# Optimization experiments

Measured on AMD Instinct MI355X. Metric: run time of the kernel, lower is better.

Reference implementation:

```python
import jax, jax.numpy as jnp
import numpy as np

K_NUM = 4      # kernel_num: size of dynamic kernel bank
KS = 3         # spatial kernel size


def _fdconv(x, w_fr, w_fi, b, a1w, a1b, a2w, a2b):
    """Frequency-dynamic conv: kernels parameterized in the Fourier domain,
    mixed per-sample by a GAP->MLP->softmax attention over the kernel bank,
    then applied as a per-sample 3x3 conv (batched via grouped conv).
    x: [B,Cin,H,W]; w_fr/w_fi: [K,Cout,Cin,3,2] (rfft2 coeffs); b: [Cout]."""
    B, Cin, H, W = x.shape
    # per-sample kernel attention
    gap = x.mean((2, 3))                                   # [B,Cin]
    h = jax.nn.relu(gap @ a1w + a1b)                       # [B,hidden]
    attn = jax.nn.softmax(h @ a2w + a2b, axis=-1)          # [B,K]
    # synthesize spatial kernels from frequency coefficients
    w = jnp.fft.irfft2(w_fr + 1j * w_fi, s=(KS, KS), axes=(-2, -1))  # [K,Co,Ci,3,3]
    w = w.astype(x.dtype)
    wd = jnp.einsum('bk,koihw->boihw', attn, w)            # [B,Co,Ci,3,3]
    Co = wd.shape[1]
    # per-sample conv via feature_group_count=B grouped conv
    xg = x.reshape(1, B * Cin, H, W)
    wg = wd.reshape(B * Co, Cin, KS, KS)
    y = jax.lax.conv_general_dilated(
        xg, wg, window_strides=(1, 1), padding='SAME',
        dimension_numbers=('NCHW', 'OIHW', 'NCHW'),
        feature_group_count=B)
    return y.reshape(B, Co, H, W) + b[None, :, None, None]


def setup_inputs() -> dict:
    key = jax.random.key(0)
    ks = jax.random.split(key, 16)
    B, Cin, Cout, H, W = 16, 128, 256, 128, 128
    h1, h2 = Cin // 4, Cout // 4
    FR = KS // 2 + 1  # rfft bins along last dim
    s = 0.05
    return {
        'x': jax.random.normal(ks[0], (B, Cin, H, W), jnp.float32),
        # conv1 (Cin->Cout)
        'w1_fr': jax.random.normal(ks[1], (K_NUM, Cout, Cin, KS, FR), jnp.float32) * s,
        'w1_fi': jax.random.normal(ks[2], (K_NUM, Cout, Cin, KS, FR), jnp.float32) * s,
        'b1': jnp.zeros((Cout,), jnp.float32),
        'a1w1': jax.random.normal(ks[3], (Cin, h1), jnp.float32) * s,
        'a1b1': jnp.zeros((h1,), jnp.float32),
        'a1w2': jax.random.normal(ks[4], (h1, K_NUM), jnp.float32) * s,
        'a1b2': jnp.zeros((K_NUM,), jnp.float32),
        # conv2 (Cout->Cout)
        'w2_fr': jax.random.normal(ks[5], (K_NUM, Cout, Cout, KS, FR), jnp.float32) * s,
        'w2_fi': jax.random.normal(ks[6], (K_NUM, Cout, Cout, KS, FR), jnp.float32) * s,
        'b2': jnp.zeros((Cout,), jnp.float32),
        'a2w1': jax.random.normal(ks[7], (Cout, h2), jnp.float32) * s,
        'a2b1': jnp.zeros((h2,), jnp.float32),
        'a2w2': jax.random.normal(ks[8], (h2, K_NUM), jnp.float32) * s,
        'a2b2': jnp.zeros((K_NUM,), jnp.float32),
    }


def reference(x, w1_fr, w1_fi, b1, a1w1, a1b1, a1w2, a1b2,
              w2_fr, w2_fi, b2, a2w1, a2b1, a2w2, a2b2):
    y = jax.nn.relu(_fdconv(x, w1_fr, w1_fi, b1, a1w1, a1b1, a1w2, a1b2))
    y = jax.nn.relu(_fdconv(y, w2_fr, w2_fi, b2, a2w1, a2b1, a2w2, a2b2))
    return y
```

## Files before the change

### kernel.cpp

```cpp
#include <hip/hip_runtime.h>
#include <hip/hip_bf16.h>
#include <math.h>


#define K_NUM 4
typedef __attribute__((ext_vector_type(8))) short short8;
typedef __attribute__((ext_vector_type(4))) float f32x4;

__device__ inline float bf2f(short s) {
  unsigned u = ((unsigned)(unsigned short)s) << 16;
  return __uint_as_float(u);
}
__device__ inline short f2bf(float f) {
  __hip_bfloat16 h = __float2bfloat16(f);
  return (short)*reinterpret_cast<unsigned short*>(&h);
}

__global__ __launch_bounds__(256) void gap_reduce_kernel(
    const float* __restrict__ part, float* __restrict__ gap, float scale, int n4) {
  int row = blockIdx.x * 4 + (threadIdx.x >> 6);
  int lane = threadIdx.x & 63;
  float4 v = {0.f, 0.f, 0.f, 0.f};
  if (lane < n4) v = *(const float4*)(part + (size_t)row * 256 + lane * 4);
  float s = v.x + v.y + v.z + v.w;
#pragma unroll
  for (int m = 1; m <= 32; m <<= 1) s += __shfl_xor(s, m, 64);
  if (lane == 0) gap[row] = s * scale;
}

__global__ void fd_attn_kernel(const float* __restrict__ gap, int C, int Hd,
                               const float* __restrict__ w1, const float* __restrict__ b1,
                               const float* __restrict__ w2, const float* __restrict__ b2,
                               float* __restrict__ attn) {
  int b = blockIdx.x, j = threadIdx.x;
  __shared__ float h[64];
  __shared__ float z[K_NUM];
  if (j < Hd) {
    float s = b1[j];
    const float* g = gap + (size_t)b * C;
    for (int c = 0; c < C; ++c) s = fmaf(g[c], w1[c * Hd + j], s);
    h[j] = fmaxf(s, 0.f);
  }
  __syncthreads();
  if (j < K_NUM) {
    float s = b2[j];
    for (int c = 0; c < Hd; ++c) s = fmaf(h[c], w2[c * K_NUM + j], s);
    z[j] = s;
  }
  __syncthreads();
  if (j == 0) {
    float m = z[0];
    for (int k = 1; k < K_NUM; ++k) m = fmaxf(m, z[k]);
    float e[K_NUM], sum = 0.f;
    for (int k = 0; k < K_NUM; ++k) { e[k] = expf(z[k] - m); sum += e[k]; }
    for (int k = 0; k < K_NUM; ++k) attn[b * K_NUM + k] = e[k] / sum;
  }
}

__global__ void fd_synth_t_kernel(const float* __restrict__ wfr, const float* __restrict__ wfi,
                                  const float* __restrict__ attn, short* __restrict__ wdt,
                                  int B, int CO, int CI) {
  size_t gid = (size_t)blockIdx.x * blockDim.x + threadIdx.x;
  size_t total = (size_t)B * CI * CO;
  if (gid >= total) return;
  int ci = (int)(gid % CI);
  size_t t = gid / CI;
  int co = (int)(t % CO);
  int b = (int)(t / CO);

  float a[K_NUM];
  for (int k = 0; k < K_NUM; ++k) a[k] = attn[b * K_NUM + k];

  float Fr[3][2], Fi[3][2];
  for (int u = 0; u < 3; ++u) for (int v = 0; v < 2; ++v) { Fr[u][v] = 0.f; Fi[u][v] = 0.f; }
  for (int k = 0; k < K_NUM; ++k) {
    size_t base = ((((size_t)k * CO + co) * CI + ci) * 3) * 2;
    const float* pr = wfr + base;
    const float* pi = wfi + base;
    float ak = a[k];
    for (int u = 0; u < 3; ++u)
      for (int v = 0; v < 2; ++v) {
        Fr[u][v] = fmaf(ak, pr[u * 2 + v], Fr[u][v]);
        Fi[u][v] = fmaf(ak, pi[u * 2 + v], Fi[u][v]);
      }
  }

  const float CS[3] = {1.f, -0.5f, -0.5f};
  const float SN[3] = {0.f, 0.8660254037844386f, -0.8660254037844386f};
  float outv[9];
  for (int ai = 0; ai < 3; ++ai) {
    float Gr[2], Gi[2];
    for (int v = 0; v < 2; ++v) {
      float gr = 0.f, gi = 0.f;
      for (int u = 0; u < 3; ++u) {
        int idx = (u * ai) % 3;
        gr += Fr[u][v] * CS[idx] - Fi[u][v] * SN[idx];
        gi += Fr[u][v] * SN[idx] + Fi[u][v] * CS[idx];
      }
      Gr[v] = gr * (1.f / 3.f);
      Gi[v] = gi * (1.f / 3.f);
    }
    for (int bi = 0; bi < 3; ++bi)
      outv[ai * 3 + bi] = (Gr[0] + 2.f * (Gr[1] * CS[bi] - Gi[1] * SN[bi])) * (1.f / 3.f);
  }
  int ci8 = ci >> 3, cil = ci & 7;
  for (int s = 0; s < 9; ++s)
    wdt[((((size_t)b * 9 + s) * (CI / 8) + ci8) * CO + co) * 8 + cil] = f2bf(outv[s]);
}

__global__ __launch_bounds__(256) void transpose_bf16_kernel(
    const float* __restrict__ in, short* __restrict__ out, int C,
    float* __restrict__ gpart1) {
  const int HW = 16384;
  __shared__ short t[64 * 40];
  int tid = threadIdx.x;
  int px0 = blockIdx.x * 64, c0 = blockIdx.y * 32, b = blockIdx.z;
  int px = tid & 63, cb = tid >> 6;
  float sums[8];
#pragma unroll
  for (int i = 0; i < 8; ++i) {
    int c = i * 4 + cb;
    float v = in[((size_t)b * C + c0 + c) * HW + px0 + px];
    t[px * 40 + c] = f2bf(v);
    sums[i] = v;
  }
  __syncthreads();
  int px2 = tid >> 2, g = tid & 3;
  short8 v = *(const short8*)(t + px2 * 40 + g * 8);
  *(short8*)(out + ((size_t)b * HW + px0 + px2) * C + c0 + g * 8) = v;
#pragma unroll
  for (int m = 1; m <= 32; m <<= 1)
#pragma unroll
    for (int i = 0; i < 8; ++i) sums[i] += __shfl_xor(sums[i], m, 64);
  if ((tid & 63) == 0)
#pragma unroll
    for (int i = 0; i < 8; ++i)
      gpart1[((size_t)b * C + c0 + i * 4 + cb) * 256 + blockIdx.x] = sums[i];
}

template <int CI, int MODE>
__global__ __launch_bounds__(512, 2) void conv_mfma_kernel(
    const short* __restrict__ xin,
    const short* __restrict__ wdt,
    const float* __restrict__ bias,
    short* __restrict__ yout_t,
    float* __restrict__ yout_f,
    float* __restrict__ gpart2) {
  const int H = 128, W = 128, HW = H * W, CO = 256;
  const int NKC = CI / 32;
  __shared__ short xs[2][18 * 18 * 40];

  const int tid = threadIdx.x;
  const int w = tid >> 6;
  const int wy = w & 1, wc = w >> 1;
  const int lane = tid & 63;
  const int l15 = lane & 15, l4 = lane >> 4;
  const int tx0 = (blockIdx.x & 7) * 16, ty0 = (blockIdx.x >> 3) * 16;
  const int cob = wc * 64;
  const int b = blockIdx.z;

  int sr[3], sc[3], sg[3];
#pragma unroll
  for (int i = 0; i < 3; ++i) {
    int idx = i * 512 + tid;
    int pxi = idx >> 2;
    sg[i] = idx & 3;
    sr[i] = pxi / 18;
    sc[i] = pxi - sr[i] * 18;
  }
  const bool has2 = (tid < 272);

  short8 pre[3];
  auto stage_load = [&](int kc) {
#pragma unroll
    for (int i = 0; i < 3; ++i) {
      if (i < 2 || has2) {
        int gy = ty0 + sr[i] - 1, gx = tx0 + sc[i] - 1;
        short8 v = {0, 0, 0, 0, 0, 0, 0, 0};
        if ((unsigned)gy < (unsigned)H && (unsigned)gx < (unsigned)W)
          v = *(const short8*)(xin + ((size_t)b * HW + gy * W + gx) * CI + kc * 32 + sg[i] * 8);
        pre[i] = v;
      }
    }
  };
  auto stage_write = [&](short* buf) {
#pragma unroll
    for (int i = 0; i < 3; ++i) {
      if (i < 2 || has2) {
        int pxi = sr[i] * 18 + sc[i];
        *(short8*)(buf + pxi * 40 + sg[i] * 8) = pre[i];
      }
    }
  };

  f32x4 acc[8][4];
#pragma unroll
  for (int i = 0; i < 8; ++i)
#pragma unroll
    for (int j = 0; j < 4; ++j)
      acc[i][j] = (f32x4){0.f, 0.f, 0.f, 0.f};

  stage_load(0);
  stage_write(xs[0]);
  __syncthreads();

  int cur = 0;
  for (int kc = 0; kc < NKC; ++kc) {
    const bool more = (kc + 1 < NKC);
    if (more) stage_load(kc + 1);
    const short* bufc = xs[cur];

#pragma unroll
    for (int dc = 0; dc < 3; ++dc) {
      short8 xf[10];
#pragma unroll
      for (int rr = 0; rr < 10; ++rr)
        xf[rr] = *(const short8*)(bufc + ((8 * wy + rr) * 18 + l15 + dc) * 40 + l4 * 8);
#pragma unroll
      for (int dr = 0; dr < 3; ++dr) {
        short8 wf[4];
        const short* wp = wdt + ((((size_t)b * 9 + dr * 3 + dc) * (CI / 8) + kc * 4 + l4) * CO + cob + l15) * 8;
#pragma unroll
        for (int cf = 0; cf < 4; ++cf)
          wf[cf] = *(const short8*)(wp + cf * 128);
#pragma unroll
        for (int nf = 0; nf < 8; ++nf)
#pragma unroll
          for (int cf = 0; cf < 4; ++cf) {
            if (MODE == 0)
              acc[nf][cf] = __builtin_amdgcn_mfma_f32_16x16x32_bf16(
                  xf[nf + dr], wf[cf], acc[nf][cf], 0, 0, 0);
            else
              acc[nf][cf] = __builtin_amdgcn_mfma_f32_16x16x32_bf16(
                  wf[cf], xf[nf + dr], acc[nf][cf], 0, 0, 0);
          }
      }
    }

    if (more) stage_write(xs[cur ^ 1]);
    __syncthreads();
    cur ^= 1;
  }

  if (MODE == 0) {
    float gs[4];
#pragma unroll
    for (int cf = 0; cf < 4; ++cf) gs[cf] = 0.f;
#pragma unroll
    for (int cf = 0; cf < 4; ++cf) {
      float bs = bias[cob + cf * 16 + l15];
#pragma unroll
      for (int nf = 0; nf < 8; ++nf) {
        int row = ty0 + 8 * wy + nf;
#pragma unroll
        for (int r = 0; r < 4; ++r) {
          int col = tx0 + l4 * 4 + r;
          float v = fmaxf(acc[nf][cf][r] + bs, 0.f);
          gs[cf] += v;
          yout_t[((size_t)b * HW + (size_t)row * W + col) * CO + cob + cf * 16 + l15] = f2bf(v);
        }
      }
    }
#pragma unroll
    for (int cf = 0; cf < 4; ++cf) {
      gs[cf] += __shfl_xor(gs[cf], 16, 64);
      gs[cf] += __shfl_xor(gs[cf], 32, 64);
    }
    if (l4 == 0) {
      int pslot = blockIdx.x * 2 + wy;
#pragma unroll
      for (int cf = 0; cf < 4; ++cf)
        gpart2[((size_t)b * 256 + cob + cf * 16 + l15) * 256 + pslot] = gs[cf];
    }
  } else {
#pragma unroll
    for (int cf = 0; cf < 4; ++cf) {
#pragma unroll
      for (int r = 0; r < 4; ++r) {
        int co = cob + cf * 16 + l4 * 4 + r;
        float bs = bias[co];
#pragma unroll
        for (int nf = 0; nf < 8; ++nf) {
          int row = ty0 + 8 * wy + nf;
          int col = tx0 + l15;
          yout_f[((size_t)b * CO + co) * HW + (size_t)row * W + col] =
              fmaxf(acc[nf][cf][r] + bs, 0.f);
        }
      }
    }
  }
}

extern "C" void kernel_launch(void* const* d_in, const int* in_sizes, int n_in,
                              void* d_out, int out_size, void* d_ws, size_t ws_size,
                              hipStream_t stream) {
  const int B = 16, CIN = 128, COUT = 256, H = 128, W = 128, HW = H * W;

  const float* x    = (const float*)d_in[0];
  const float* w1fr = (const float*)d_in[1];
  const float* w1fi = (const float*)d_in[2];
  const float* b1   = (const float*)d_in[3];
  const float* a1w1 = (const float*)d_in[4];
  const float* a1b1 = (const float*)d_in[5];
  const float* a1w2 = (const float*)d_in[6];
  const float* a1b2 = (const float*)d_in[7];
  const float* w2fr = (const float*)d_in[8];
  const float* w2fi = (const float*)d_in[9];
  const float* b2   = (const float*)d_in[10];
  const float* a2w1 = (const float*)d_in[11];
  const float* a2b1 = (const float*)d_in[12];
  const float* a2w2 = (const float*)d_in[13];
  const float* a2b2 = (const float*)d_in[14];
  float* outf = (float*)d_out;

  short* xt     = (short*)d_out;
  float* gpart1 = (float*)((char*)d_out + 67108864);
  float* gpart2 = (float*)((char*)d_out + 69206016);

  char* wsb = (char*)d_ws;
  short* y1t  = (short*)wsb;
  short* wdt  = (short*)(wsb + 134217728);
  float* gap1 = (float*)(wsb + 134217728 + 18874368);
  float* gap2 = (float*)(wsb + 134217728 + 18874368 + 8192);
  float* attn = (float*)(wsb + 134217728 + 18874368 + 8192 + 16384);

  const float gsc = 1.f / (float)HW;

  transpose_bf16_kernel<<<dim3(HW / 64, CIN / 32, B), 256, 0, stream>>>(x, xt, CIN, gpart1);
  gap_reduce_kernel<<<(B * CIN) / 4, 256, 0, stream>>>(gpart1, gap1, gsc, 64);
  fd_attn_kernel<<<B, 64, 0, stream>>>(gap1, CIN, CIN / 4, a1w1, a1b1, a1w2, a1b2, attn);
  fd_synth_t_kernel<<<(B * CIN * COUT) / 256, 256, 0, stream>>>(w1fr, w1fi, attn, wdt, B, COUT, CIN);
  conv_mfma_kernel<128, 0><<<dim3(64, 1, 16), 512, 0, stream>>>(xt, wdt, b1, y1t, nullptr, gpart2);

  gap_reduce_kernel<<<(B * COUT) / 4, 256, 0, stream>>>(gpart2, gap2, gsc, 32);
  fd_attn_kernel<<<B, 64, 0, stream>>>(gap2, COUT, COUT / 4, a2w1, a2b1, a2w2, a2b2, attn);
  fd_synth_t_kernel<<<(B * COUT * COUT) / 256, 256, 0, stream>>>(w2fr, w2fi, attn, wdt, B, COUT, COUT);
  conv_mfma_kernel<256, 1><<<dim3(64, 1, 16), 512, 0, stream>>>(y1t, wdt, b2, nullptr, outf, nullptr);
}
```

Baseline: 925.6 us.

## Switch conv to 32x32x16 MFMA with 32x8 tiles and channel-group-major LDS layout

Reworks the per-sample conv kernel to use 32x32x16 bf16 MFMA instead of 16x16x32. The spatial tile changes from 16x16 to 32 wide by 8 high. Shared memory becomes channel-group-major with a padded pixel stride, and staging is simplified to one pixel per thread. The larger MFMA shape is meant to raise operand reuse and cut LDS reads and issue overhead per FLOP. In exchange, the halo overhead of the wider, shorter tile grows, and the new LDS pattern may cause bank conflicts.

After: 1.015 ms. +9.6%, slower.

```diff
diff --git a/kernel.cpp b/kernel.cpp
--- a/kernel.cpp
+++ b/kernel.cpp
@@ -6,6 +6,7 @@
 #define K_NUM 4
 typedef __attribute__((ext_vector_type(8))) short short8;
 typedef __attribute__((ext_vector_type(4))) float f32x4;
+typedef __attribute__((ext_vector_type(16))) float f32x16;
 
 __device__ inline float bf2f(short s) {
   unsigned u = ((unsigned)(unsigned short)s) << 16;
@@ -148,57 +149,51 @@
     float* __restrict__ gpart2) {
   const int H = 128, W = 128, HW = H * W, CO = 256;
   const int NKC = CI / 32;
-  __shared__ short xs[2][18 * 18 * 40];
+  const int NPX = 340;
+  const int NPXP = 346;
+  __shared__ short xs[2][4 * NPXP * 8];
 
   const int tid = threadIdx.x;
   const int w = tid >> 6;
   const int wy = w & 1, wc = w >> 1;
   const int lane = tid & 63;
-  const int l15 = lane & 15, l4 = lane >> 4;
-  const int tx0 = (blockIdx.x & 7) * 16, ty0 = (blockIdx.x >> 3) * 16;
+  const int l31 = lane & 31;
+  const int h = lane >> 5;
+  const int tx0 = (blockIdx.x & 3) * 32, ty0 = (blockIdx.x >> 2) * 8;
   const int cob = wc * 64;
   const int b = blockIdx.z;
 
-  int sr[3], sc[3], sg[3];
-#pragma unroll
-  for (int i = 0; i < 3; ++i) {
-    int idx = i * 512 + tid;
-    int pxi = idx >> 2;
-    sg[i] = idx & 3;
-    sr[i] = pxi / 18;
-    sc[i] = pxi - sr[i] * 18;
-  }
-  const bool has2 = (tid < 272);
-
-  short8 pre[3];
+  const int sp = tid;
+  const int srr = sp / 34, scc = sp - srr * 34;
+  const int sgy = ty0 + srr - 1, sgx = tx0 + scc - 1;
+  const bool sok = (tid < NPX);
+  const bool sin = sok && (unsigned)sgy < (unsigned)H && (unsigned)sgx < (unsigned)W;
+  const short* sgp = xin + ((size_t)b * HW + sgy * W + sgx) * CI;
+
+  short8 pre[4];
   auto stage_load = [&](int kc) {
 #pragma unroll
-    for (int i = 0; i < 3; ++i) {
-      if (i < 2 || has2) {
-        int gy = ty0 + sr[i] - 1, gx = tx0 + sc[i] - 1;
-        short8 v = {0, 0, 0, 0, 0, 0, 0, 0};
-        if ((unsigned)gy < (unsigned)H && (unsigned)gx < (unsigned)W)
-          v = *(const short8*)(xin + ((size_t)b * HW + gy * W + gx) * CI + kc * 32 + sg[i] * 8);
-        pre[i] = v;
-      }
+    for (int g = 0; g < 4; ++g) {
+      short8 v = {0, 0, 0, 0, 0, 0, 0, 0};
+      if (sin) v = *(const short8*)(sgp + kc * 32 + g * 8);
+      pre[g] = v;
     }
   };
   auto stage_write = [&](short* buf) {
-#pragma unroll
-    for (int i = 0; i < 3; ++i) {
-      if (i < 2 || has2) {
-        int pxi = sr[i] * 18 + sc[i];
-        *(short8*)(buf + pxi * 40 + sg[i] * 8) = pre[i];
-      }
+    if (sok) {
+#pragma unroll
+      for (int g = 0; g < 4; ++g)
+        *(short8*)(buf + (g * NPXP + sp) * 8) = pre[g];
     }
   };
 
-  f32x4 acc[8][4];
-#pragma unroll
-  for (int i = 0; i < 8; ++i)
-#pragma unroll
-    for (int j = 0; j < 4; ++j)
-      acc[i][j] = (f32x4){0.f, 0.f, 0.f, 0.f};
+  f32x16 acc[4][2];
+#pragma unroll
+  for (int i = 0; i < 4; ++i)
+#pragma unroll
+    for (int j = 0; j < 2; ++j)
+#pragma unroll
+      for (int r = 0; r < 16; ++r) acc[i][j][r] = 0.f;
 
   stage_load(0);
   stage_write(xs[0]);
@@ -212,28 +207,33 @@
 
 #pragma unroll
     for (int dc = 0; dc < 3; ++dc) {
-      short8 xf[10];
-#pragma unroll
-      for (int rr = 0; rr < 10; ++rr)
-        xf[rr] = *(const short8*)(bufc + ((8 * wy + rr) * 18 + l15 + dc) * 40 + l4 * 8);
-#pragma unroll
-      for (int dr = 0; dr < 3; ++dr) {
-        short8 wf[4];
-        const short* wp = wdt + ((((size_t)b * 9 + dr * 3 + dc) * (CI / 8) + kc * 4 + l4) * CO + cob + l15) * 8;
-#pragma unroll
-        for (int cf = 0; cf < 4; ++cf)
-          wf[cf] = *(const short8*)(wp + cf * 128);
-#pragma unroll
-        for (int nf = 0; nf < 8; ++nf)
-#pragma unroll
-          for (int cf = 0; cf < 4; ++cf) {
-            if (MODE == 0)
-              acc[nf][cf] = __builtin_amdgcn_mfma_f32_16x16x32_bf16(
-                  xf[nf + dr], wf[cf], acc[nf][cf], 0, 0, 0);
-            else
-              acc[nf][cf] = __builtin_amdgcn_mfma_f32_16x16x32_bf16(
-                  wf[cf], xf[nf + dr], acc[nf][cf], 0, 0, 0);
-          }
+#pragma unroll
+      for (int ks = 0; ks < 2; ++ks) {
+        short8 xf[6];
+#pragma unroll
+        for (int rr = 0; rr < 6; ++rr) {
+          int p = (wy * 4 + rr) * 34 + l31 + dc;
+          xf[rr] = *(const short8*)(bufc + ((ks * 2 + h) * NPXP + p) * 8);
+        }
+#pragma unroll
+        for (int dr = 0; dr < 3; ++dr) {
+          short8 wf[2];
+          const short* wp = wdt + ((((size_t)b * 9 + dr * 3 + dc) * (CI / 8) + kc * 4 + ks * 2 + h) * CO + cob + l31) * 8;
+#pragma unroll
+          for (int ncf = 0; ncf < 2; ++ncf)
+            wf[ncf] = *(const short8*)(wp + ncf * 32 * 8);
+#pragma unroll
+          for (int nf = 0; nf < 4; ++nf)
+#pragma unroll
+            for (int ncf = 0; ncf < 2; ++ncf) {
+              if (MODE == 0)
+                acc[nf][ncf] = __builtin_amdgcn_mfma_f32_32x32x16_bf16(
+                    xf[nf + dr], wf[ncf], acc[nf][ncf], 0, 0, 0);
+              else
+                acc[nf][ncf] = __builtin_amdgcn_mfma_f32_32x32x16_bf16(
+                    wf[ncf], xf[nf + dr], acc[nf][ncf], 0, 0, 0);
+            }
+        }
       }
     }
 
@@ -243,48 +243,44 @@
   }
 
   if (MODE == 0) {
-    float gs[4];
-#pragma unroll
-    for (int cf = 0; cf < 4; ++cf) gs[cf] = 0.f;
-#pragma unroll
-    for (int cf = 0; cf < 4; ++cf) {
-      float bs = bias[cob + cf * 16 + l15];
-#pragma unroll
-      for (int nf = 0; nf < 8; ++nf) {
-        int row = ty0 + 8 * wy + nf;
-#pragma unroll
-        for (int r = 0; r < 4; ++r) {
-          int col = tx0 + l4 * 4 + r;
-          float v = fmaxf(acc[nf][cf][r] + bs, 0.f);
-          gs[cf] += v;
-          yout_t[((size_t)b * HW + (size_t)row * W + col) * CO + cob + cf * 16 + l15] = f2bf(v);
+    float gs[2] = {0.f, 0.f};
+#pragma unroll
+    for (int ncf = 0; ncf < 2; ++ncf) {
+      int co = cob + ncf * 32 + l31;
+      float bs = bias[co];
+#pragma unroll
+      for (int nf = 0; nf < 4; ++nf) {
+        int row = ty0 + wy * 4 + nf;
+#pragma unroll
+        for (int reg = 0; reg < 16; ++reg) {
+          int mcol = (reg & 3) + 8 * (reg >> 2) + 4 * h;
+          int col = tx0 + mcol;
+          float v = fmaxf(acc[nf][ncf][reg] + bs, 0.f);
+          gs[ncf] += v;
+          yout_t[((size_t)b * HW + (size_t)row * W + col) * CO + co] = f2bf(v);
         }
       }
     }
 #pragma unroll
-    for (int cf = 0; cf < 4; ++cf) {
-      gs[cf] += __shfl_xor(gs[cf], 16, 64);
-      gs[cf] += __shfl_xor(gs[cf], 32, 64);
-    }
-    if (l4 == 0) {
+    for (int ncf = 0; ncf < 2; ++ncf) gs[ncf] += __shfl_xor(gs[ncf], 32, 64);
+    if (lane < 32) {
       int pslot = blockIdx.x * 2 + wy;
 #pragma unroll
-      for (int cf = 0; cf < 4; ++cf)
-        gpart2[((size_t)b * 256 + cob + cf * 16 + l15) * 256 + pslot] = gs[cf];
+      for (int ncf = 0; ncf < 2; ++ncf)
+        gpart2[((size_t)b * 256 + cob + ncf * 32 + lane) * 256 + pslot] = gs[ncf];
     }
   } else {
 #pragma unroll
-    for (int cf = 0; cf < 4; ++cf) {
-#pragma unroll
-      for (int r = 0; r < 4; ++r) {
-        int co = cob + cf * 16 + l4 * 4 + r;
+    for (int ncf = 0; ncf < 2; ++ncf) {
+#pragma unroll
+      for (int reg = 0; reg < 16; ++reg) {
+        int co = cob + ncf * 32 + (reg & 3) + 8 * (reg >> 2) + 4 * h;
         float bs = bias[co];
 #pragma unroll
-        for (int nf = 0; nf < 8; ++nf) {
-          int row = ty0 + 8 * wy + nf;
-          int col = tx0 + l15;
-          yout_f[((size_t)b * CO + co) * HW + (size_t)row * W + col] =
-              fmaxf(acc[nf][cf][r] + bs, 0.f);
+        for (int nf = 0; nf < 4; ++nf) {
+          int row = ty0 + wy * 4 + nf;
+          yout_f[((size_t)b * CO + co) * HW + (size_t)row * W + tx0 + l31] =
+              fmaxf(acc[nf][ncf][reg] + bs, 0.f);
         }
       }
     }
```
